# Optimization experiments

Hardware: AMD Instinct MI355X
Metric: run time of the kernel (lower is better)

Reference implementation:

```python
import jax, jax.numpy as jnp
import numpy as np

NUM_HEADS = 16

def setup_inputs() -> dict:
    key = jax.random.key(0)
    k1, k2, k3 = jax.random.split(key, 3)
    B, N, C = 2, 2048, 1024
    x = jax.random.normal(k1, (B, N, C), dtype=jnp.float32)
    Wqkv = jax.random.normal(k2, (3 * C, C), dtype=jnp.float32) * (C ** -0.5)
    Wproj = jax.random.normal(k3, (C, C), dtype=jnp.float32) * (C ** -0.5)
    bproj = jnp.zeros((C,), dtype=jnp.float32)
    return {"x": x, "Wqkv": Wqkv, "Wproj": Wproj, "bproj": bproj}

def reference(x, Wqkv, Wproj, bproj):
    B, N, C = x.shape
    H = NUM_HEADS
    D = C // H
    scale = D ** -0.5
    # torch Linear: y = x @ W^T ; qkv -> [B,N,3,H,D]
    qkv = (x @ Wqkv.T).reshape(B, N, 3, H, D)
    q = qkv[:, :, 0].transpose(0, 2, 1, 3)  # [B,H,N,D]
    k = qkv[:, :, 1].transpose(0, 2, 1, 3)
    v = qkv[:, :, 2].transpose(0, 2, 1, 3)
    attn = jnp.einsum('bhnd,bhmd->bhnm', q, k) * scale  # [B,H,N,N]
    attn = jax.nn.softmax(attn, axis=-1)
    out = jnp.einsum('bhnm,bhmd->bhnd', attn, v)  # [B,H,N,D]
    out = out.transpose(0, 2, 1, 3).reshape(B, N, C)
    return out @ Wproj.T + bproj
```

## Files before the change

### kernel.cpp

```cpp
#include <hip/hip_runtime.h>

typedef unsigned short u16;
typedef unsigned int u32;
typedef __attribute__((ext_vector_type(8))) short short8;
typedef __attribute__((ext_vector_type(8))) __bf16 bf16x8;
typedef __attribute__((ext_vector_type(4))) float f32x4;
typedef __attribute__((ext_vector_type(16))) float f32x16;
typedef __attribute__((ext_vector_type(4))) unsigned short us4;
typedef __attribute__((ext_vector_type(4))) unsigned int u32x4;

#define DEVFN static __device__ __forceinline__

DEVFN u16 f2bf(float f) {
  u32 u = __float_as_uint(f);
  return (u16)((u + 0x7fffu + ((u >> 16) & 1u)) >> 16);
}

#if __has_builtin(__builtin_amdgcn_exp2f)
DEVFN float fexp2(float x) { return __builtin_amdgcn_exp2f(x); }
#else
DEVFN float fexp2(float x) { return exp2f(x); }
#endif

template <typename T>
DEVFN auto mfma16_imp(T a, T b, f32x4 c, int)
    -> decltype(__builtin_amdgcn_mfma_f32_16x16x32_bf16(a, b, c, 0, 0, 0)) {
  return __builtin_amdgcn_mfma_f32_16x16x32_bf16(a, b, c, 0, 0, 0);
}
template <typename T>
DEVFN f32x4 mfma16_imp(T a, T b, f32x4 c, long) {
  return __builtin_amdgcn_mfma_f32_16x16x32_bf16(
      __builtin_bit_cast(bf16x8, a), __builtin_bit_cast(bf16x8, b), c, 0, 0, 0);
}
DEVFN f32x4 MFMA(short8 a, short8 b, f32x4 c) { return mfma16_imp(a, b, c, 0); }

template <typename T>
DEVFN auto mfma32_imp(T a, T b, f32x16 c, int)
    -> decltype(__builtin_amdgcn_mfma_f32_32x32x16_bf16(a, b, c, 0, 0, 0)) {
  return __builtin_amdgcn_mfma_f32_32x32x16_bf16(a, b, c, 0, 0, 0);
}
template <typename T>
DEVFN f32x16 mfma32_imp(T a, T b, f32x16 c, long) {
  return __builtin_amdgcn_mfma_f32_32x32x16_bf16(
      __builtin_bit_cast(bf16x8, a), __builtin_bit_cast(bf16x8, b), c, 0, 0, 0);
}
DEVFN f32x16 MFMA32(short8 a, short8 b, f32x16 c) { return mfma32_imp(a, b, c, 0); }

DEVFN void gload_lds16(const u16* g, u16* l) {
  __builtin_amdgcn_global_load_lds(
      (__attribute__((address_space(1))) void*)g,
      (__attribute__((address_space(3))) void*)l, 16, 0, 0);
}

DEVFN u32 cvtpk_bf16(float lo, float hi) {
  u32 w;
  asm("v_cvt_pk_bf16_f32 %0, %1, %2" : "=v"(w) : "v"(lo), "v"(hi));
  return w;
}

__global__ void __launch_bounds__(256) cvt_all(
    const float* __restrict__ x, u16* __restrict__ xo,
    const float* __restrict__ w1, u16* __restrict__ w1o,
    const float* __restrict__ w2, u16* __restrict__ w2o) {
  int bid = blockIdx.x;
  const float* in;
  u16* out;
  int i;
  if (bid < 4096) {
    in = x; out = xo; i = bid * 256 + threadIdx.x;
  } else if (bid < 7168) {
    in = w1; out = w1o; i = (bid - 4096) * 256 + threadIdx.x;
  } else {
    in = w2; out = w2o; i = (bid - 7168) * 256 + threadIdx.x;
  }
  f32x4 v = ((const f32x4*)in)[i];
  us4 o;
  o[0] = f2bf(v[0]); o[1] = f2bf(v[1]); o[2] = f2bf(v[2]); o[3] = f2bf(v[3]);
  ((us4*)out)[i] = o;
}

template <int F32OUT, int BN>
DEVFN void gemm_tile(const u16* __restrict__ A, const u16* __restrict__ Bm,
                     u16* __restrict__ Cbf, float* __restrict__ Cf,
                     const float* __restrict__ bias, int N, int K, int bm,
                     int bn, u16* As, u16* Bs) {
  const int tid = threadIdx.x;
  const int wave = tid >> 6, lane = tid & 63;
  const int wr = (wave >> 1) * 64, wc = (wave & 1) * (BN / 2);
  const int srow = lane >> 2, scol = (lane & 3) * 8;
  const int fr = lane & 15, fk = (lane >> 4) * 8;
  const int NB = BN / 64;
  const int NI = BN / 32;

  f32x4 acc[4][NI] = {};

  for (int k0 = 0; k0 < K; k0 += 32) {
    __syncthreads();
#pragma unroll
    for (int t = 0; t < 2; ++t) {
      int rr = (wave * 2 + t) * 16 + srow;
      gload_lds16(A + (size_t)(bm + rr) * K + k0 + scol, As + (wave * 2 + t) * 512);
    }
#pragma unroll
    for (int t = 0; t < NB; ++t) {
      int rr = (wave * NB + t) * 16 + srow;
      gload_lds16(Bm + (size_t)(bn + rr) * K + k0 + scol, Bs + (wave * NB + t) * 512);
    }
    __syncthreads();
    short8 af[4], bf[NI];
#pragma unroll
    for (int i = 0; i < 4; ++i)
      af[i] = *(const short8*)(As + (wr + i * 16 + fr) * 32 + fk);
#pragma unroll
    for (int i = 0; i < NI; ++i)
      bf[i] = *(const short8*)(Bs + (wc + i * 16 + fr) * 32 + fk);
#pragma unroll
    for (int mi = 0; mi < 4; ++mi)
#pragma unroll
      for (int ni = 0; ni < NI; ++ni)
        acc[mi][ni] = MFMA(af[mi], bf[ni], acc[mi][ni]);
  }

  const int orow = (lane >> 4) * 4, ocol = lane & 15;
#pragma unroll
  for (int mi = 0; mi < 4; ++mi)
#pragma unroll
    for (int ni = 0; ni < NI; ++ni)
#pragma unroll
      for (int r = 0; r < 4; ++r) {
        size_t row = (size_t)(bm + wr + mi * 16 + orow + r);
        size_t col = (size_t)(bn + wc + ni * 16 + ocol);
        if (F32OUT)
          Cf[row * N + col] = acc[mi][ni][r] + bias[col];
        else
          Cbf[row * N + col] = f2bf(acc[mi][ni][r]);
      }
}

__global__ void __launch_bounds__(256) gemm_proj(
    const u16* __restrict__ A, const u16* __restrict__ Bm,
    float* __restrict__ Cf, const float* __restrict__ bias, int M, int N,
    int K) {
  __shared__ u16 As[128 * 32];
  __shared__ u16 Bs[64 * 32];
  gemm_tile<1, 64>(A, Bm, nullptr, Cf, bias, N, K, blockIdx.x * 128,
                   blockIdx.y * 64, As, Bs);
}

__global__ void __launch_bounds__(256) fused_qkv_gemm(
    const u16* __restrict__ x, const u16* __restrict__ wqkv,
    u16* __restrict__ qk, u16* __restrict__ vt) {
  __shared__ u16 As[128 * 32];
  __shared__ u16 Bs[128 * 32];
  int bid = blockIdx.x;
  if (bid < 512) {
    gemm_tile<0, 128>(x, wqkv, qk, nullptr, nullptr, 2048, 1024,
                      (bid & 31) * 128, (bid >> 5) * 128, As, Bs);
  } else {
    int j = bid - 512;
    gemm_tile<0, 128>(wqkv + (size_t)2048 * 1024, x, vt, nullptr, nullptr,
                      4096, 1024, (j & 7) * 128, (j >> 3) * 128, As, Bs);
  }
}

__global__ void __launch_bounds__(512) attn_kernel(const u16* __restrict__ qk,
                                                   const u16* __restrict__ vT,
                                                   u16* __restrict__ attn_out) {
  __shared__ u16 SM[32768];

  const int tid = threadIdx.x;
  const int wave = tid >> 6, lane = tid & 63;
  const int g = wave >> 2, gw = wave & 3;
  const int q5 = lane & 31, hi = lane >> 5;
  const int qb = blockIdx.x, h = blockIdx.y, b = blockIdx.z;
  const size_t tok0 = (size_t)b * 2048;
  const float SCALE = 0.18033688011112042f;

  u16* const Kg = SM + g * 2 * 4096;
  u16* const Vg = SM + 16384 + g * 2 * 4096;
  const int kvoff = g * 1024;

  const size_t qrow = tok0 + qb * 128 + gw * 32 + q5;
  const u16* qp = qk + qrow * 2048 + h * 64 + hi * 8;
  short8 qf[4];
#pragma unroll
  for (int ks = 0; ks < 4; ++ks) qf[ks] = *(const short8*)(qp + ks * 16);

  const u16* kbase = qk + tok0 * 2048 + 1024 + h * 64;
  const u16* vtb = vT + (size_t)h * 64 * 4096 + tok0;

  const int rowl = lane >> 3;
  const int k_srcoff = ((lane & 7) ^ rowl) * 8;

  float m_run = -1e30f, l_run = 0.f;
  f32x16 o0 = {}, o1 = {};

#define STAGE(kv0, buf)                                                        \
  {                                                                            \
    _Pragma("unroll") for (int c = 0; c < 2; ++c) {                            \
      int rw = c * 4 + gw;                                                     \
      int row = rw * 8 + rowl;                                                 \
      gload_lds16(kbase + (size_t)((kv0) + row) * 2048 + k_srcoff,             \
                  Kg + (buf) * 4096 + rw * 512);                               \
      int vso = (((lane & 7) ^ rowl ^ rw) * 8);    \
      gload_lds16(vtb + (size_t)row * 4096 + (kv0) + vso,                      \
                  Vg + (buf) * 4096 + rw * 512);                               \
    }                                                                          \
  }

  STAGE(kvoff, 0);
  __syncthreads();

  for (int t = 0; t < 16; ++t) {
    const int cur = t & 1, nxt = cur ^ 1;
    if (t < 15) STAGE(kvoff + (t + 1) * 64, nxt);

    const u16* Kc = Kg + cur * 4096;
    f32x16 s0 = {}, s1 = {};
    __builtin_amdgcn_s_setprio(1);
#pragma unroll
    for (int ks = 0; ks < 4; ++ks) {
      int ch = ((ks * 2 + hi) ^ (q5 & 7)) * 8;
      short8 k0 = *(const short8*)(Kc + q5 * 64 + ch);
      short8 k1 = *(const short8*)(Kc + (32 + q5) * 64 + ch);
      s0 = MFMA32(k0, qf[ks], s0);
      s1 = MFMA32(k1, qf[ks], s1);
    }
    __builtin_amdgcn_s_setprio(0);

    float mt[8];
#pragma unroll
    for (int i = 0; i < 8; ++i)
      mt[i] = fmaxf(fmaxf(s0[i], s0[i + 8]), fmaxf(s1[i], s1[i + 8]));
    float pmax = fmaxf(fmaxf(fmaxf(mt[0], mt[1]), fmaxf(mt[2], mt[3])),
                       fmaxf(fmaxf(mt[4], mt[5]), fmaxf(mt[6], mt[7])));
    pmax = fmaxf(pmax, __shfl_xor(pmax, 32, 64));
    float mraw = pmax * SCALE;

    if (__any(mraw > m_run + 8.f)) {
      float mn = fmaxf(m_run, mraw);
      float alpha = fexp2(m_run - mn);
#pragma unroll
      for (int i = 0; i < 16; ++i) { o0[i] *= alpha; o1[i] *= alpha; }
      l_run *= alpha;
      m_run = mn;
    }

    float p0[16], p1[16];
    float rs = 0.f;
#pragma unroll
    for (int i = 0; i < 16; ++i) {
      p0[i] = fexp2(fmaf(s0[i], SCALE, -m_run));
      p1[i] = fexp2(fmaf(s1[i], SCALE, -m_run));
      rs += p0[i] + p1[i];
    }
    rs += __shfl_xor(rs, 32, 64);
    l_run += rs;

    u32 w0[4][2], w1[4][2];
#pragma unroll
    for (int a = 0; a < 4; ++a) {
      w0[a][0] = cvtpk_bf16(p0[4 * a], p0[4 * a + 1]);
      w0[a][1] = cvtpk_bf16(p0[4 * a + 2], p0[4 * a + 3]);
      w1[a][0] = cvtpk_bf16(p1[4 * a], p1[4 * a + 1]);
      w1[a][1] = cvtpk_bf16(p1[4 * a + 2], p1[4 * a + 3]);
    }
    short8 pb[4];
#pragma unroll
    for (int ks = 0; ks < 4; ++ks) {
      int e = ks & 1;
      u32 x0 = (ks < 2) ? w0[2 * e][0] : w1[2 * e][0];
      u32 y0 = (ks < 2) ? w0[2 * e + 1][0] : w1[2 * e + 1][0];
      u32 x1 = (ks < 2) ? w0[2 * e][1] : w1[2 * e][1];
      u32 y1 = (ks < 2) ? w0[2 * e + 1][1] : w1[2 * e + 1][1];
      asm("v_permlane32_swap_b32 %0, %1" : "+v"(x0), "+v"(y0));
      asm("v_permlane32_swap_b32 %0, %1" : "+v"(x1), "+v"(y1));
      u32x4 tt = {x0, x1, y0, y1};
      pb[ks] = __builtin_bit_cast(short8, tt);
    }

    const u16* Vc = Vg + cur * 4096;
    __builtin_amdgcn_s_setprio(1);
#pragma unroll
    for (int ks = 0; ks < 4; ++ks) {
      int ch0 = ((ks * 2 + hi) ^ (q5 & 7) ^ ((q5 >> 3) & 7)) * 8;
      int ch1 = ch0 ^ (4 * 8);
      short8 v0 = *(const short8*)(Vc + q5 * 64 + ch0);
      short8 v1 = *(const short8*)(Vc + (32 + q5) * 64 + ch1);
      o0 = MFMA32(v0, pb[ks], o0);
      o1 = MFMA32(v1, pb[ks], o1);
    }
    __builtin_amdgcn_s_setprio(0);

    __syncthreads();
  }
#undef STAGE

  float* sm = (float*)SM;
  float* base = sm + gw * 2176;
  if (g == 1) {
    base[lane] = m_run;
    base[64 + lane] = l_run;
#pragma unroll
    for (int i = 0; i < 16; ++i) {
      base[128 + i * 64 + lane] = o0[i];
      base[128 + (16 + i) * 64 + lane] = o1[i];
    }
  }
  __syncthreads();
  if (g == 0) {
    float m1 = base[lane], l1 = base[64 + lane];
    float M = fmaxf(m_run, m1);
    float wa = fexp2(m_run - M), wb = fexp2(m1 - M);
    float inv = 1.f / (wa * l_run + wb * l1);
#pragma unroll
    for (int dt = 0; dt < 2; ++dt)
#pragma unroll
      for (int gq = 0; gq < 4; ++gq) {
        us4 st;
#pragma unroll
        for (int c2 = 0; c2 < 4; ++c2) {
          int i = 4 * gq + c2;
          float mine = (dt == 0) ? o0[i] : o1[i];
          float oth = base[128 + (dt * 16 + i) * 64 + lane];
          st[c2] = f2bf((wa * mine + wb * oth) * inv);
        }
        int col = h * 64 + dt * 32 + 8 * gq + 4 * hi;
        *(us4*)(attn_out + qrow * 1024 + col) = st;
      }
  }
}

extern "C" void kernel_launch(void* const* d_in, const int* in_sizes, int n_in,
                              void* d_out, int out_size, void* d_ws, size_t ws_size,
                              hipStream_t stream) {
  const float* x = (const float*)d_in[0];
  const float* Wqkv = (const float*)d_in[1];
  const float* Wproj = (const float*)d_in[2];
  const float* bproj = (const float*)d_in[3];
  float* out = (float*)d_out;

  char* ws = (char*)d_ws;
  u16* x_bf     = (u16*)(ws);
  u16* wqkv_bf  = (u16*)(ws + 8388608);
  u16* wproj_bf = (u16*)(ws + 14680064);
  u16* qk_bf    = (u16*)(ws + 16777216);
  u16* vt_bf    = (u16*)(ws + 33554432);
  u16* attn_bf  = (u16*)(ws + 41943040);

  cvt_all<<<8192, 256, 0, stream>>>(x, x_bf, Wqkv, wqkv_bf, Wproj, wproj_bf);

  fused_qkv_gemm<<<768, 256, 0, stream>>>(x_bf, wqkv_bf, qk_bf, vt_bf);

  dim3 g2(16, 16, 2);
  attn_kernel<<<g2, 512, 0, stream>>>(qk_bf, vt_bf, attn_bf);

  dim3 g3(32, 16);
  gemm_proj<<<g3, 256, 0, stream>>>(attn_bf, wproj_bf, out, bproj,
                                    4096, 1024, 1024);
}
```

Baseline: 121.8 us.

## Read K/V fragments directly from global memory instead of LDS staging

Removes the double-buffered LDS staging of K and V tiles and their per-iteration barriers. Each lane now loads its K and V MFMA operands straight from global memory, relying on the cache, and LDS is kept only for the final combine of the two wave groups. This drops the LDS traffic and synchronisation, but each wave now issues uncoalesced global loads and the four waves in a group re-read the same K/V data with no prefetch overlap.

```diff
diff --git a/kernel.cpp b/kernel.cpp
--- a/kernel.cpp
+++ b/kernel.cpp
@@ -166,7 +166,7 @@
 __global__ void __launch_bounds__(512) attn_kernel(const u16* __restrict__ qk,
                                                    const u16* __restrict__ vT,
                                                    u16* __restrict__ attn_out) {
-  __shared__ u16 SM[32768];
+  __shared__ float CMB[4 * 2176];
 
   const int tid = threadIdx.x;
   const int wave = tid >> 6, lane = tid & 63;
@@ -175,9 +175,6 @@
   const int qb = blockIdx.x, h = blockIdx.y, b = blockIdx.z;
   const size_t tok0 = (size_t)b * 2048;
   const float SCALE = 0.18033688011112042f;
-
-  u16* const Kg = SM + g * 2 * 4096;
-  u16* const Vg = SM + 16384 + g * 2 * 4096;
   const int kvoff = g * 1024;
 
   const size_t qrow = tok0 + qb * 128 + gw * 32 + q5;
@@ -186,43 +183,22 @@
 #pragma unroll
   for (int ks = 0; ks < 4; ++ks) qf[ks] = *(const short8*)(qp + ks * 16);
 
-  const u16* kbase = qk + tok0 * 2048 + 1024 + h * 64;
-  const u16* vtb = vT + (size_t)h * 64 * 4096 + tok0;
-
-  const int rowl = lane >> 3;
-  const int k_srcoff = ((lane & 7) ^ rowl) * 8;
+  const u16* kp = qk + (tok0 + 1024 * 0 ) * 0;
+  kp = qk + tok0 * 2048 + 1024 + h * 64 + (size_t)(kvoff + q5) * 2048 + hi * 8;
+  const u16* vp = vT + (size_t)h * 64 * 4096 + tok0 + (size_t)q5 * 4096 +
+                  kvoff + hi * 8;
 
   float m_run = -1e30f, l_run = 0.f;
   f32x16 o0 = {}, o1 = {};
 
-#define STAGE(kv0, buf)                                                        \
-  {                                                                            \
-    _Pragma("unroll") for (int c = 0; c < 2; ++c) {                            \
-      int rw = c * 4 + gw;                                                     \
-      int row = rw * 8 + rowl;                                                 \
-      gload_lds16(kbase + (size_t)((kv0) + row) * 2048 + k_srcoff,             \
-                  Kg + (buf) * 4096 + rw * 512);                               \
-      int vso = (((lane & 7) ^ rowl ^ rw) * 8);    \
-      gload_lds16(vtb + (size_t)row * 4096 + (kv0) + vso,                      \
-                  Vg + (buf) * 4096 + rw * 512);                               \
-    }                                                                          \
-  }
-
-  STAGE(kvoff, 0);
-  __syncthreads();
-
   for (int t = 0; t < 16; ++t) {
-    const int cur = t & 1, nxt = cur ^ 1;
-    if (t < 15) STAGE(kvoff + (t + 1) * 64, nxt);
-
-    const u16* Kc = Kg + cur * 4096;
+    const u16* kt = kp + (size_t)t * (64 * 2048);
     f32x16 s0 = {}, s1 = {};
     __builtin_amdgcn_s_setprio(1);
 #pragma unroll
     for (int ks = 0; ks < 4; ++ks) {
-      int ch = ((ks * 2 + hi) ^ (q5 & 7)) * 8;
-      short8 k0 = *(const short8*)(Kc + q5 * 64 + ch);
-      short8 k1 = *(const short8*)(Kc + (32 + q5) * 64 + ch);
+      short8 k0 = *(const short8*)(kt + ks * 16);
+      short8 k1 = *(const short8*)(kt + 65536 + ks * 16);
       s0 = MFMA32(k0, qf[ks], s0);
       s1 = MFMA32(k1, qf[ks], s1);
     }
@@ -279,25 +255,19 @@
       pb[ks] = __builtin_bit_cast(short8, tt);
     }
 
-    const u16* Vc = Vg + cur * 4096;
+    const u16* vt_ = vp + t * 64;
     __builtin_amdgcn_s_setprio(1);
 #pragma unroll
     for (int ks = 0; ks < 4; ++ks) {
-      int ch0 = ((ks * 2 + hi) ^ (q5 & 7) ^ ((q5 >> 3) & 7)) * 8;
-      int ch1 = ch0 ^ (4 * 8);
-      short8 v0 = *(const short8*)(Vc + q5 * 64 + ch0);
-      short8 v1 = *(const short8*)(Vc + (32 + q5) * 64 + ch1);
+      short8 v0 = *(const short8*)(vt_ + ks * 16);
+      short8 v1 = *(const short8*)(vt_ + 131072 + ks * 16);
       o0 = MFMA32(v0, pb[ks], o0);
       o1 = MFMA32(v1, pb[ks], o1);
     }
     __builtin_amdgcn_s_setprio(0);
-
-    __syncthreads();
-  }
-#undef STAGE
-
-  float* sm = (float*)SM;
-  float* base = sm + gw * 2176;
+  }
+
+  float* base = CMB + gw * 2176;
   if (g == 1) {
     base[lane] = m_run;
     base[64 + lane] = l_run;
```

Result: slower. 193.5 us (+58.8%).
